# Optimization experiments

Hardware: AMD Instinct MI355X
Metric: run time of the kernel (lower is better)

The kernel has to match this reference:

```python
import jax, jax.numpy as jnp
import numpy as np
from jax import lax

B, T, HID = 2, 2048, 2048
H, DK, DV = 16, 64, 128          # num_heads, head_k_dim, head_v_dim
C = 16                            # chunk_size (hardcoded in module __call__)
LOWR = 16                         # gate_low_rank_dim
NORMALIZER = 16.0                 # gate_logit_normalizer
EPS = 1e-5
SCALE = DK ** -0.5


def setup_inputs() -> dict:
    key = jax.random.key(0)
    ks = jax.random.split(key, 9)
    def w(k, shape):
        return jax.random.normal(k, shape, jnp.float32) * (shape[0] ** -0.5)
    return {
        "hidden_states": jax.random.normal(ks[0], (B, T, HID), jnp.float32),
        "Wq": w(ks[1], (HID, H * DK)),
        "Wk": w(ks[2], (HID, H * DK)),
        "Wv": w(ks[3], (HID, H * DV)),
        "Wg": w(ks[4], (HID, H * DV)),
        "Wgk1": w(ks[5], (HID, LOWR)),
        "Wgk2": w(ks[6], (LOWR, H * DK)),
        "bgk2": jnp.zeros((H * DK,), jnp.float32),
        "Wo": w(ks[7], (H * DV, HID)),
        "norm_w": jnp.ones((DV,), jnp.float32),
    }


def _chunk_gla(q, k, v, gk):
    """Chunked gated linear attention.
    q,k,gk: [B,T,H,DK], v: [B,T,H,DV]; gk is log-decay (<= 0).
    Recurrence: S_t = diag(exp(gk_t)) S_{t-1} + k_t^T v_t ; o_t = scale * q_t S_t.
    """
    b, t, h, dk = q.shape
    dv = v.shape[-1]
    n = t // C
    def to_chunks(x):  # [B,T,H,d] -> [B,H,N,C,d]
        return x.reshape(b, n, C, h, x.shape[-1]).transpose(0, 3, 1, 2, 4)
    q, k, v, gk = map(to_chunks, (q, k, v, gk))

    gc = jnp.cumsum(gk, axis=3)                 # within-chunk cumulative log-decay
    qe = q * jnp.exp(gc) * SCALE                # decay-weighted queries
    ke = k * jnp.exp(-gc)                       # inverse-decay keys (safe for C=16)
    # intra-chunk causal attention: A[i,j] = sum_d q_i k_j exp(gc_i - gc_j), j<=i
    A = jnp.einsum('bhncd,bhnmd->bhncm', qe, ke)
    A = jnp.where(jnp.tril(jnp.ones((C, C), bool)), A, 0.0)
    o_intra = jnp.einsum('bhncm,bhnme->bhnce', A, v)

    g_last = gc[:, :, :, -1:, :]                # [B,H,N,1,DK]
    k_dec = k * jnp.exp(g_last - gc)            # keys decayed to end of chunk
    kv = jnp.einsum('bhncd,bhnce->bhnde', k_dec, v)   # per-chunk state increment
    decay = jnp.exp(g_last[:, :, :, 0, :])      # [B,H,N,DK] total chunk decay

    def step(S, inp):  # S: [B,H,DK,DV]
        qe_c, kv_c, dec_c = inp
        o_c = jnp.einsum('bhcd,bhde->bhce', qe_c, S)
        return dec_c[..., None] * S + kv_c, o_c

    S0 = jnp.zeros((b, h, dk, dv), q.dtype)
    xs = (qe.transpose(2, 0, 1, 3, 4), kv.transpose(2, 0, 1, 3, 4), decay.transpose(2, 0, 1, 3))
    _, o_inter = lax.scan(step, S0, xs)          # [N,B,H,C,DV]

    o = o_intra + o_inter.transpose(1, 2, 0, 3, 4)
    return o.transpose(0, 2, 3, 1, 4).reshape(b, t, h, dv)  # [B,T,H,DV]


def reference(hidden_states, Wq, Wk, Wv, Wg, Wgk1, Wgk2, bgk2, Wo, norm_w):
    x = hidden_states
    q = (x @ Wq).reshape(B, T, H, DK)
    k = (x @ Wk).reshape(B, T, H, DK)
    v = (x @ Wv).reshape(B, T, H, DV)
    gk = jax.nn.log_sigmoid((x @ Wgk1) @ Wgk2 + bgk2) / NORMALIZER
    gk = gk.reshape(B, T, H, DK)

    o = _chunk_gla(q, k, v, gk)                  # [B,T,H,DV]

    # FusedRMSNormGated: rmsnorm(o) * weight, gated by swish(g) per head
    g = (x @ Wg).reshape(B, T, H, DV)
    o = o * lax.rsqrt(jnp.mean(o * o, axis=-1, keepdims=True) + EPS) * norm_w
    o = o * (g * jax.nn.sigmoid(g))
    return o.reshape(B, T, H * DV) @ Wo
```

## Files before the change

kernel.cpp:

```cpp
#include <hip/hip_runtime.h>
#include <hip/hip_bf16.h>
#include <math.h>

#define B_    2
#define T_    2048
#define HID_  2048
#define H_    16
#define DK_   64
#define DV_   128
#define CC    16
#define NCHUNK (T_/CC)
#define NSEG  16
#define M_    (B_*T_)
#define SCALE_ 0.125f

typedef __attribute__((ext_vector_type(8))) __bf16 bf16x8;
typedef __attribute__((ext_vector_type(4))) float f32x4;

__device__ __forceinline__ unsigned short f2bf(float f) {
  unsigned int u = __float_as_uint(f);
  u += 0x7fff + ((u >> 16) & 1);
  return (unsigned short)(u >> 16);
}
__device__ __forceinline__ float bf2f(unsigned short u) {
  return __uint_as_float(((unsigned int)u) << 16);
}

typedef const __attribute__((address_space(1))) void* as1cv;
typedef __attribute__((address_space(3))) void* as3v;
__device__ __forceinline__ void gload16(const void* g, void* l) {
  __builtin_amdgcn_global_load_lds((as1cv)g, (as3v)l, 16, 0, 0);
}

__global__ __launch_bounds__(256) void prep_kernel(const float* __restrict__ x,
                                                   unsigned short* __restrict__ xb,
                                                   const float* __restrict__ Wq,
                                                   const float* __restrict__ Wk,
                                                   const float* __restrict__ Wv,
                                                   const float* __restrict__ Wg,
                                                   const float* __restrict__ Wo,
                                                   unsigned short* __restrict__ WqkT,
                                                   unsigned short* __restrict__ WvgT,
                                                   unsigned short* __restrict__ WoT) {
  int id = blockIdx.x;
  if (id < 8192) {
    int i = id * 256 + threadIdx.x;
    float4 f = reinterpret_cast<const float4*>(x)[i];
    ushort4 u;
    u.x = f2bf(f.x); u.y = f2bf(f.y); u.z = f2bf(f.z); u.w = f2bf(f.w);
    reinterpret_cast<ushort4*>(xb)[i] = u;
    return;
  }
  id -= 8192;
  const float* in; unsigned short* out; int N;
  if (id < 2048)       { in = Wq; out = WqkT;                         N = 1024; }
  else if (id < 4096)  { in = Wk; out = WqkT + (size_t)1024*2048;     N = 1024; id -= 2048; }
  else if (id < 8192)  { in = Wv; out = WvgT;                         N = 2048; id -= 4096; }
  else if (id < 12288) { in = Wg; out = WvgT + (size_t)2048*2048;     N = 2048; id -= 8192; }
  else                 { in = Wo; out = WoT;                          N = 2048; id -= 12288; }
  const int K = 2048;
  const int nx = N / 32;
  const int n0 = (id % nx) * 32;
  const int k0 = (id / nx) * 32;
  __shared__ float tile[32][33];
  const int tx = threadIdx.x & 31;
  const int ty = threadIdx.x >> 5;
  #pragma unroll
  for (int i = 0; i < 4; ++i)
    tile[ty + i*8][tx] = in[(size_t)(k0 + ty + i*8) * N + n0 + tx];
  __syncthreads();
  #pragma unroll
  for (int i = 0; i < 4; ++i) {
    int r = ty + i*8;
    out[(size_t)(n0 + r) * K + k0 + tx] = f2bf(tile[tx][r]);
  }
}

template<bool OBF>
__global__ __launch_bounds__(512, 2) void gemm256(const unsigned short* __restrict__ A,
                                                  const unsigned short* __restrict__ Bt,
                                                  void* __restrict__ Cv,
                                                  int M, int N, int K) {
  __shared__ char ldsb[131072];
  const int t    = threadIdx.x;
  const int lane = t & 63;
  const int wid  = t >> 6;
  const int wr   = wid >> 2;
  const int wc   = wid & 3;
  const int lr   = lane & 15;
  const int lk   = lane >> 4;
  int flat = blockIdx.y * gridDim.x + blockIdx.x;
  if (gridDim.x * gridDim.y == 256) flat = (flat & 7) * 32 + (flat >> 3);
  const int row0 = (flat / gridDim.x) * 256;
  const int col0 = (flat % gridDim.x) * 256;
  const int NKT  = K >> 6;
  const size_t K2 = (size_t)K * 2;

  const int r_s  = t >> 2;
  const int kx_s = ((t & 3) * 16) ^ (((t >> 5) & 1) << 5);

  const int ha = wr;
  const int hb = wc >> 1;
  const int rbl = (wc & 1) * 64;

  f32x4 acc[8][4];
  #pragma unroll
  for (int m = 0; m < 8; ++m)
    #pragma unroll
    for (int n = 0; n < 4; ++n) acc[m][n] = (f32x4){0.f, 0.f, 0.f, 0.f};

  auto stage_half = [&](int p, int o, int h, int kt) {
    const char* src = o ? (const char*)Bt : (const char*)A;
    const int R0 = (o ? col0 : row0) + h * 128;
    const char* g = src + (size_t)(R0 + r_s) * K2 + (size_t)kt * 128 + kx_s;
    char* l = ldsb + ((((p << 1) | o) << 1 | h) << 14) + t * 16;
    gload16(g, l);
    gload16(g + 64, l + 8192);
  };
  auto lda = [&](int p, int mf, int ks) -> bf16x8 {
    int r = mf * 16 + lr;
    int a = ((((p << 1) | 0) << 1 | ha) << 14) + ks * 8192 + r * 64 + lk * 16;
    a ^= ((r >> 3) & 1) << 5;
    return *(const bf16x8*)(ldsb + a);
  };
  auto ldb = [&](int p, int nf, int ks) -> bf16x8 {
    int r = rbl + nf * 16 + lr;
    int a = ((((p << 1) | 1) << 1 | hb) << 14) + ks * 8192 + r * 64 + lk * 16;
    a ^= ((r >> 3) & 1) << 5;
    return *(const bf16x8*)(ldsb + a);
  };

  stage_half(0, 1, 0, 0); stage_half(0, 1, 1, 0);
  stage_half(0, 0, 0, 0); stage_half(0, 0, 1, 0);
  if (1 < NKT) {
    stage_half(1, 1, 0, 1); stage_half(1, 1, 1, 1);
    stage_half(1, 0, 0, 1); stage_half(1, 0, 1, 1);
  }
  __builtin_amdgcn_sched_barrier(0);
  asm volatile("s_waitcnt vmcnt(8)" ::: "memory");
  __builtin_amdgcn_sched_barrier(0);
  __builtin_amdgcn_s_barrier();

  bf16x8 fa[4][2], fb[2][2], fb2[2][2];

  for (int kt = 0; kt < NKT; ++kt) {
    const int p = kt & 1;
    const bool st = (kt + 2 < NKT);
    #pragma unroll
    for (int m = 0; m < 4; ++m) { fa[m][0] = lda(p, m, 0); fa[m][1] = lda(p, m, 1); }
    #pragma unroll
    for (int n = 0; n < 2; ++n) { fb[n][0] = ldb(p, n, 0); fb[n][1] = ldb(p, n, 1); }
    __builtin_amdgcn_sched_barrier(0);
    __builtin_amdgcn_s_barrier();
    asm volatile("s_waitcnt lgkmcnt(0)" ::: "memory");
    __builtin_amdgcn_sched_barrier(0);
    __builtin_amdgcn_s_setprio(1);
    #pragma unroll
    for (int m = 0; m < 4; ++m)
      #pragma unroll
      for (int n = 0; n < 2; ++n) {
        acc[m][n] = __builtin_amdgcn_mfma_f32_16x16x32_bf16(fa[m][0], fb[n][0], acc[m][n], 0, 0, 0);
        acc[m][n] = __builtin_amdgcn_mfma_f32_16x16x32_bf16(fa[m][1], fb[n][1], acc[m][n], 0, 0, 0);
      }
    __builtin_amdgcn_s_setprio(0);
    __builtin_amdgcn_sched_barrier(0);
    __builtin_amdgcn_s_barrier();
    #pragma unroll
    for (int n = 0; n < 2; ++n) { fb2[n][0] = ldb(p, n + 2, 0); fb2[n][1] = ldb(p, n + 2, 1); }
    __builtin_amdgcn_sched_barrier(0);
    __builtin_amdgcn_s_barrier();
    asm volatile("s_waitcnt lgkmcnt(0)" ::: "memory");
    __builtin_amdgcn_sched_barrier(0);
    __builtin_amdgcn_s_setprio(1);
    #pragma unroll
    for (int m = 0; m < 4; ++m)
      #pragma unroll
      for (int n = 0; n < 2; ++n) {
        acc[m][n+2] = __builtin_amdgcn_mfma_f32_16x16x32_bf16(fa[m][0], fb2[n][0], acc[m][n+2], 0, 0, 0);
        acc[m][n+2] = __builtin_amdgcn_mfma_f32_16x16x32_bf16(fa[m][1], fb2[n][1], acc[m][n+2], 0, 0, 0);
      }
    __builtin_amdgcn_s_setprio(0);
    __builtin_amdgcn_sched_barrier(0);
    __builtin_amdgcn_s_barrier();
    if (st) { stage_half(p, 1, 0, kt + 2); stage_half(p, 1, 1, kt + 2); }
    #pragma unroll
    for (int m = 0; m < 4; ++m) { fa[m][0] = lda(p, m + 4, 0); fa[m][1] = lda(p, m + 4, 1); }
    __builtin_amdgcn_sched_barrier(0);
    __builtin_amdgcn_s_barrier();
    asm volatile("s_waitcnt lgkmcnt(0)" ::: "memory");
    __builtin_amdgcn_sched_barrier(0);
    __builtin_amdgcn_s_setprio(1);
    #pragma unroll
    for (int m = 0; m < 4; ++m)
      #pragma unroll
      for (int n = 0; n < 2; ++n) {
        acc[m+4][n] = __builtin_amdgcn_mfma_f32_16x16x32_bf16(fa[m][0], fb[n][0], acc[m+4][n], 0, 0, 0);
        acc[m+4][n] = __builtin_amdgcn_mfma_f32_16x16x32_bf16(fa[m][1], fb[n][1], acc[m+4][n], 0, 0, 0);
      }
    __builtin_amdgcn_s_setprio(0);
    __builtin_amdgcn_sched_barrier(0);
    __builtin_amdgcn_s_barrier();
    if (st) { stage_half(p, 0, 0, kt + 2); stage_half(p, 0, 1, kt + 2); }
    __builtin_amdgcn_sched_barrier(0);
    __builtin_amdgcn_s_setprio(1);
    #pragma unroll
    for (int m = 0; m < 4; ++m)
      #pragma unroll
      for (int n = 0; n < 2; ++n) {
        acc[m+4][n+2] = __builtin_amdgcn_mfma_f32_16x16x32_bf16(fa[m][0], fb2[n][0], acc[m+4][n+2], 0, 0, 0);
        acc[m+4][n+2] = __builtin_amdgcn_mfma_f32_16x16x32_bf16(fa[m][1], fb2[n][1], acc[m+4][n+2], 0, 0, 0);
      }
    __builtin_amdgcn_s_setprio(0);
    __builtin_amdgcn_sched_barrier(0);
    if (kt == NKT - 2) asm volatile("s_waitcnt vmcnt(0)" ::: "memory");
    else               asm volatile("s_waitcnt vmcnt(8)" ::: "memory");
    __builtin_amdgcn_sched_barrier(0);
    __builtin_amdgcn_s_barrier();
  }

  #pragma unroll
  for (int m = 0; m < 8; ++m) {
    int row = row0 + wr*128 + m*16 + lk*4;
    #pragma unroll
    for (int n = 0; n < 4; ++n) {
      int col = col0 + wc*64 + n*16 + lr;
      #pragma unroll
      for (int j = 0; j < 4; ++j) {
        if (OBF) ((unsigned short*)Cv)[(size_t)(row + j) * N + col] = f2bf(acc[m][n][j]);
        else     ((float*)Cv)[(size_t)(row + j) * N + col] = acc[m][n][j];
      }
    }
  }
}

template<bool OBF>
__global__ __launch_bounds__(512, 2) void gemm256x128(const unsigned short* __restrict__ A,
                                                      const unsigned short* __restrict__ Bt,
                                                      void* __restrict__ Cv,
                                                      int M, int N, int K) {
  __shared__ char ldsb[98304];
  const int t    = threadIdx.x;
  const int lane = t & 63;
  const int wid  = t >> 6;
  const int wr   = wid >> 1;
  const int wc   = wid & 1;
  const int lr   = lane & 15;
  const int lk   = lane >> 4;
  int flat = blockIdx.y * gridDim.x + blockIdx.x;
  if (gridDim.x * gridDim.y == 256) flat = (flat & 7) * 32 + (flat >> 3);
  const int row0 = (flat / gridDim.x) * 256;
  const int col0 = (flat % gridDim.x) * 128;
  const int NKT  = K >> 6;
  const size_t K2 = (size_t)K * 2;

  const int r_s  = t >> 2;
  const int kx_s = ((t & 3) * 16) ^ (((t >> 5) & 1) << 5);

  const int ha  = wr >> 1;
  const int ral = (wr & 1) * 64;
  const int rbl = wc * 64;

  f32x4 acc[4][4];
  #pragma unroll
  for (int m = 0; m < 4; ++m)
    #pragma unroll
    for (int n = 0; n < 4; ++n) acc[m][n] = (f32x4){0.f, 0.f, 0.f, 0.f};

  auto stage_slot = [&](int p, int slot, int kt) {
    const char* src = (slot == 2) ? (const char*)Bt : (const char*)A;
    const int R0 = (slot == 2) ? col0 : (row0 + slot * 128);
    const char* g = src + (size_t)(R0 + r_s) * K2 + (size_t)kt * 128 + kx_s;
    char* l = ldsb + p * 49152 + slot * 16384 + t * 16;
    gload16(g, l);
    gload16(g + 64, l + 8192);
  };
  auto lda = [&](int p, int mf, int ks) -> bf16x8 {
    int r = ral + mf * 16 + lr;
    int a = p * 49152 + ha * 16384 + ks * 8192 + r * 64 + lk * 16;
    a ^= ((r >> 3) & 1) << 5;
    return *(const bf16x8*)(ldsb + a);
  };
  auto ldb = [&](int p, int nf, int ks) -> bf16x8 {
    int r = rbl + nf * 16 + lr;
    int a = p * 49152 + 32768 + ks * 8192 + r * 64 + lk * 16;
    a ^= ((r >> 3) & 1) << 5;
    return *(const bf16x8*)(ldsb + a);
  };

  stage_slot(0, 2, 0); stage_slot(0, 0, 0); stage_slot(0, 1, 0);
  if (1 < NKT) { stage_slot(1, 2, 1); stage_slot(1, 0, 1); stage_slot(1, 1, 1); }
  __builtin_amdgcn_sched_barrier(0);
  asm volatile("s_waitcnt vmcnt(6)" ::: "memory");
  __builtin_amdgcn_sched_barrier(0);
  __builtin_amdgcn_s_barrier();

  bf16x8 fa[2][2], fa2[2][2], fb[2][2], fb2[2][2];

  for (int kt = 0; kt < NKT; ++kt) {
    const int p = kt & 1;
    const bool st = (kt + 2 < NKT);
    #pragma unroll
    for (int m = 0; m < 2; ++m) { fa[m][0] = lda(p, m, 0); fa[m][1] = lda(p, m, 1); }
    #pragma unroll
    for (int n = 0; n < 2; ++n) { fb[n][0] = ldb(p, n, 0); fb[n][1] = ldb(p, n, 1); }
    __builtin_amdgcn_sched_barrier(0);
    __builtin_amdgcn_s_barrier();
    asm volatile("s_waitcnt lgkmcnt(0)" ::: "memory");
    __builtin_amdgcn_sched_barrier(0);
    __builtin_amdgcn_s_setprio(1);
    #pragma unroll
    for (int m = 0; m < 2; ++m)
      #pragma unroll
      for (int n = 0; n < 2; ++n) {
        acc[m][n] = __builtin_amdgcn_mfma_f32_16x16x32_bf16(fa[m][0], fb[n][0], acc[m][n], 0, 0, 0);
        acc[m][n] = __builtin_amdgcn_mfma_f32_16x16x32_bf16(fa[m][1], fb[n][1], acc[m][n], 0, 0, 0);
      }
    __builtin_amdgcn_s_setprio(0);
    __builtin_amdgcn_sched_barrier(0);
    __builtin_amdgcn_s_barrier();
    #pragma unroll
    for (int n = 0; n < 2; ++n) { fb2[n][0] = ldb(p, n + 2, 0); fb2[n][1] = ldb(p, n + 2, 1); }
    __builtin_amdgcn_sched_barrier(0);
    __builtin_amdgcn_s_barrier();
    asm volatile("s_waitcnt lgkmcnt(0)" ::: "memory");
    __builtin_amdgcn_sched_barrier(0);
    __builtin_amdgcn_s_setprio(1);
    #pragma unroll
    for (int m = 0; m < 2; ++m)
      #pragma unroll
      for (int n = 0; n < 2; ++n) {
        acc[m][n+2] = __builtin_amdgcn_mfma_f32_16x16x32_bf16(fa[m][0], fb2[n][0], acc[m][n+2], 0, 0, 0);
        acc[m][n+2] = __builtin_amdgcn_mfma_f32_16x16x32_bf16(fa[m][1], fb2[n][1], acc[m][n+2], 0, 0, 0);
      }
    __builtin_amdgcn_s_setprio(0);
    __builtin_amdgcn_sched_barrier(0);
    __builtin_amdgcn_s_barrier();
    if (st) stage_slot(p, 2, kt + 2);
    #pragma unroll
    for (int m = 0; m < 2; ++m) { fa2[m][0] = lda(p, m + 2, 0); fa2[m][1] = lda(p, m + 2, 1); }
    __builtin_amdgcn_sched_barrier(0);
    __builtin_amdgcn_s_barrier();
    asm volatile("s_waitcnt lgkmcnt(0)" ::: "memory");
    __builtin_amdgcn_sched_barrier(0);
    __builtin_amdgcn_s_setprio(1);
    #pragma unroll
    for (int m = 0; m < 2; ++m)
      #pragma unroll
      for (int n = 0; n < 2; ++n) {
        acc[m+2][n] = __builtin_amdgcn_mfma_f32_16x16x32_bf16(fa2[m][0], fb[n][0], acc[m+2][n], 0, 0, 0);
        acc[m+2][n] = __builtin_amdgcn_mfma_f32_16x16x32_bf16(fa2[m][1], fb[n][1], acc[m+2][n], 0, 0, 0);
      }
    __builtin_amdgcn_s_setprio(0);
    __builtin_amdgcn_sched_barrier(0);
    __builtin_amdgcn_s_barrier();
    if (st) { stage_slot(p, 0, kt + 2); stage_slot(p, 1, kt + 2); }
    __builtin_amdgcn_sched_barrier(0);
    __builtin_amdgcn_s_setprio(1);
    #pragma unroll
    for (int m = 0; m < 2; ++m)
      #pragma unroll
      for (int n = 0; n < 2; ++n) {
        acc[m+2][n+2] = __builtin_amdgcn_mfma_f32_16x16x32_bf16(fa2[m][0], fb2[n][0], acc[m+2][n+2], 0, 0, 0);
        acc[m+2][n+2] = __builtin_amdgcn_mfma_f32_16x16x32_bf16(fa2[m][1], fb2[n][1], acc[m+2][n+2], 0, 0, 0);
      }
    __builtin_amdgcn_s_setprio(0);
    __builtin_amdgcn_sched_barrier(0);
    if (kt == NKT - 2) asm volatile("s_waitcnt vmcnt(0)" ::: "memory");
    else               asm volatile("s_waitcnt vmcnt(6)" ::: "memory");
    __builtin_amdgcn_sched_barrier(0);
    __builtin_amdgcn_s_barrier();
  }

  #pragma unroll
  for (int m = 0; m < 4; ++m) {
    int row = row0 + wr*64 + m*16 + lk*4;
    #pragma unroll
    for (int n = 0; n < 4; ++n) {
      int col = col0 + wc*64 + n*16 + lr;
      #pragma unroll
      for (int j = 0; j < 4; ++j) {
        if (OBF) ((unsigned short*)Cv)[(size_t)(row + j) * N + col] = f2bf(acc[m][n][j]);
        else     ((float*)Cv)[(size_t)(row + j) * N + col] = acc[m][n][j];
      }
    }
  }
}

__global__ __launch_bounds__(256) void lr_kernel(const float* __restrict__ x,
                                                 const float* __restrict__ w1,
                                                 const float* __restrict__ w2,
                                                 const float* __restrict__ bias,
                                                 float* __restrict__ gkout) {
  __shared__ float part[16][17];
  __shared__ float tr[16];
  const int row = blockIdx.x;
  const int j = threadIdx.x & 15;
  const int p = threadIdx.x >> 4;
  const float* xr = x + (size_t)row * HID_;
  float acc = 0.f;
  const int k0 = p * 128;
  for (int kk = k0; kk < k0 + 128; kk += 4) {
    float4 xv = *reinterpret_cast<const float4*>(&xr[kk]);
    acc = fmaf(xv.x, w1[(kk+0)*16 + j], acc);
    acc = fmaf(xv.y, w1[(kk+1)*16 + j], acc);
    acc = fmaf(xv.z, w1[(kk+2)*16 + j], acc);
    acc = fmaf(xv.w, w1[(kk+3)*16 + j], acc);
  }
  part[p][j] = acc;
  __syncthreads();
  if (threadIdx.x < 16) {
    float s = 0.f;
    #pragma unroll
    for (int pp = 0; pp < 16; ++pp) s += part[pp][threadIdx.x];
    tr[threadIdx.x] = s;
  }
  __syncthreads();
  for (int n = threadIdx.x; n < H_*DK_; n += 256) {
    float a2 = bias[n];
    #pragma unroll
    for (int jj = 0; jj < 16; ++jj) a2 = fmaf(tr[jj], w2[jj * (H_*DK_) + n], a2);
    float ls = fminf(a2, 0.f) - log1pf(expf(-fabsf(a2)));
    gkout[(size_t)row * (H_*DK_) + n] = ls * (1.f / 16.f);
  }
}

__global__ __launch_bounds__(256) void gla_phase_a(const float* __restrict__ qk,
                                                   const unsigned short* __restrict__ vg,
                                                   const float* __restrict__ gk,
                                                   float* __restrict__ Sseg,
                                                   float* __restrict__ Dseg) {
  const int seg = blockIdx.x & 15;
  const int h   = (blockIdx.x >> 4) & 15;
  const int b   = blockIdx.x >> 8;
  const int t    = threadIdx.x;
  const int lane = t & 63;
  const int wid  = t >> 6;
  const int q    = lane >> 4;
  const int lr   = lane & 15;
  __shared__ float gc[16][68];
  __shared__ float dec_[64];
  __shared__ unsigned short kdT[64][40];
  __shared__ unsigned short vvT[128][40];

  for (int i = t; i < 1024; i += 256) kdT[i >> 4][16 + (i & 15)] = 0;
  for (int i = t; i < 2048; i += 256) vvT[i >> 4][16 + (i & 15)] = 0;

  f32x4 s_reg[2][4];
  #pragma unroll
  for (int et = 0; et < 2; ++et)
    #pragma unroll
    for (int dt = 0; dt < 4; ++dt) s_reg[et][dt] = (f32x4){0.f,0.f,0.f,0.f};
  float gt = 0.f;

  for (int c8 = 0; c8 < NCHUNK/NSEG; ++c8) {
    const int ch = seg * (NCHUNK/NSEG) + c8;
    __syncthreads();
    {
      float acc = 0.f;
      #pragma unroll
      for (int c = 0; c < CC; ++c) {
        acc += gk[((size_t)(b*T_ + ch*CC + c)) * 1024 + h*DK_ + lane];
        gc[c][lane] = acc;
      }
      gt += acc;
      dec_[lane] = expf(acc);
    }
    __syncthreads();
    {
      int c = t >> 4, d0 = (t & 15) * 4;
      float4 k4 = *reinterpret_cast<const float4*>(
          &qk[((size_t)(b*T_ + ch*CC + c)) * 2048 + 1024 + h*DK_ + d0]);
      float ka[4] = {k4.x, k4.y, k4.z, k4.w};
      #pragma unroll
      for (int j = 0; j < 4; ++j)
        kdT[d0 + j][c] = f2bf(ka[j] * expf(gc[CC-1][d0 + j] - gc[c][d0 + j]));
    }
    {
      int c = t & 15, e0 = (t >> 4) * 8;
      const ushort4* vp = reinterpret_cast<const ushort4*>(
          &vg[((size_t)(b*T_ + ch*CC + c)) * 4096 + h*DV_ + e0]);
      ushort4 a = vp[0], bb = vp[1];
      vvT[e0+0][c] = a.x;  vvT[e0+1][c] = a.y;  vvT[e0+2][c] = a.z;  vvT[e0+3][c] = a.w;
      vvT[e0+4][c] = bb.x; vvT[e0+5][c] = bb.y; vvT[e0+6][c] = bb.z; vvT[e0+7][c] = bb.w;
    }
    __syncthreads();
    bf16x8 vf[2], kf[4];
    #pragma unroll
    for (int et = 0; et < 2; ++et)
      vf[et] = *(const bf16x8*)&vvT[wid*32 + et*16 + lr][q*8];
    #pragma unroll
    for (int dt = 0; dt < 4; ++dt)
      kf[dt] = *(const bf16x8*)&kdT[dt*16 + lr][q*8];
    #pragma unroll
    for (int et = 0; et < 2; ++et)
      #pragma unroll
      for (int dt = 0; dt < 4; ++dt) {
        f32x4 dl = __builtin_amdgcn_mfma_f32_16x16x32_bf16(vf[et], kf[dt],
                     (f32x4){0.f,0.f,0.f,0.f}, 0, 0, 0);
        float dv = dec_[dt*16 + lr];
        #pragma unroll
        for (int j = 0; j < 4; ++j)
          s_reg[et][dt][j] = fmaf(s_reg[et][dt][j], dv, dl[j]);
      }
  }
  const size_t base = ((size_t)((b*H_ + h)*NSEG + seg)) * (DK_*DV_);
  #pragma unroll
  for (int et = 0; et < 2; ++et)
    #pragma unroll
    for (int dt = 0; dt < 4; ++dt)
      #pragma unroll
      for (int j = 0; j < 4; ++j)
        Sseg[base + (size_t)(wid*32 + et*16 + q*4 + j) * 64 + dt*16 + lr] = s_reg[et][dt][j];
  if (t < 64)
    Dseg[(size_t)((b*H_ + h)*NSEG + seg) * DK_ + t] = expf(gt);
}

__global__ __launch_bounds__(256) void gla_combine(float* __restrict__ Sseg,
                                                   const float* __restrict__ Dseg) {
  const int bh = blockIdx.x;
  const int t = threadIdx.x;
  __shared__ float Dl[64];
  float4 S_run[8];
  #pragma unroll
  for (int j = 0; j < 8; ++j) S_run[j] = (float4){0.f,0.f,0.f,0.f};
  const int d0 = (t * 4) & 63;
  for (int seg = 0; seg < NSEG; ++seg) {
    const size_t base = ((size_t)bh*NSEG + seg) * (DK_*DV_);
    if (t < 64) Dl[t] = Dseg[((size_t)bh*NSEG + seg) * DK_ + t];
    __syncthreads();
    #pragma unroll
    for (int j = 0; j < 8; ++j) {
      int idx = j*1024 + t*4;
      float4 sl = *reinterpret_cast<float4*>(&Sseg[base + idx]);
      *reinterpret_cast<float4*>(&Sseg[base + idx]) = S_run[j];
      S_run[j].x = fmaf(Dl[d0+0], S_run[j].x, sl.x);
      S_run[j].y = fmaf(Dl[d0+1], S_run[j].y, sl.y);
      S_run[j].z = fmaf(Dl[d0+2], S_run[j].z, sl.z);
      S_run[j].w = fmaf(Dl[d0+3], S_run[j].w, sl.w);
    }
    __syncthreads();
  }
}

__global__ __launch_bounds__(256) void gla_phase_c(const float* __restrict__ qk,
                                                   const unsigned short* __restrict__ vg,
                                                   const float* __restrict__ gk,
                                                   const float* __restrict__ Sseg,
                                                   const float* __restrict__ norm_w,
                                                   unsigned short* __restrict__ yb) {
  const int seg = blockIdx.x & 15;
  const int h   = (blockIdx.x >> 4) & 15;
  const int b   = blockIdx.x >> 8;
  const int t    = threadIdx.x;
  const int lane = t & 63;
  const int wid  = t >> 6;
  const int q    = lane >> 4;
  const int lr   = lane & 15;
  __shared__ float gc[16][68];
  __shared__ float dec_[64];
  __shared__ unsigned short qe[16][72];
  __shared__ unsigned short ke[16][72];
  __shared__ unsigned short kdT[64][40];
  __shared__ unsigned short vvT[128][40];
  __shared__ unsigned short Am[16][40];
  __shared__ unsigned short Sb[128][72];
  __shared__ float ss_lds[4][16];
  __shared__ float nw[128];

  for (int i = t; i < 1024; i += 256) kdT[i >> 4][16 + (i & 15)] = 0;
  for (int i = t; i < 2048; i += 256) vvT[i >> 4][16 + (i & 15)] = 0;
  if (t < 256) { int c = t >> 4, m = t & 15; Am[c][16 + m] = 0; }
  if (t < 128) nw[t] = norm_w[t];

  f32x4 s_reg[2][4];
  const size_t sbase = ((size_t)((b*H_ + h)*NSEG + seg)) * (DK_*DV_);
  #pragma unroll
  for (int et = 0; et < 2; ++et)
    #pragma unroll
    for (int dt = 0; dt < 4; ++dt)
      #pragma unroll
      for (int j = 0; j < 4; ++j) {
        int e = wid*32 + et*16 + q*4 + j, d = dt*16 + lr;
        float v = Sseg[sbase + (size_t)e * 64 + d];
        s_reg[et][dt][j] = v;
        Sb[e][d] = f2bf(v);
      }

  for (int c8 = 0; c8 < NCHUNK/NSEG; ++c8) {
    const int ch = seg * (NCHUNK/NSEG) + c8;
    __syncthreads();
    {
      float acc = 0.f;
      #pragma unroll
      for (int c = 0; c < CC; ++c) {
        acc += gk[((size_t)(b*T_ + ch*CC + c)) * 1024 + h*DK_ + lane];
        gc[c][lane] = acc;
      }
      dec_[lane] = expf(acc);
    }
    __syncthreads();
    {
      int c = t >> 4, d0 = (t & 15) * 4;
      const size_t gbq = ((size_t)(b*T_ + ch*CC + c)) * 2048 + h*DK_ + d0;
      float4 q4 = *reinterpret_cast<const float4*>(&qk[gbq]);
      float4 k4 = *reinterpret_cast<const float4*>(&qk[gbq + 1024]);
      float qa[4] = {q4.x, q4.y, q4.z, q4.w};
      float ka[4] = {k4.x, k4.y, k4.z, k4.w};
      ushort4 qw, kw;
      unsigned short* qwp = (unsigned short*)&qw;
      unsigned short* kwp = (unsigned short*)&kw;
      #pragma unroll
      for (int j = 0; j < 4; ++j) {
        float gcv = gc[c][d0 + j];
        float gl  = gc[CC-1][d0 + j];
        qwp[j] = f2bf(qa[j] * expf(gcv) * SCALE_);
        kwp[j] = f2bf(ka[j] * expf(-gcv));
        kdT[d0 + j][c] = f2bf(ka[j] * expf(gl - gcv));
      }
      *reinterpret_cast<ushort4*>(&qe[c][d0]) = qw;
      *reinterpret_cast<ushort4*>(&ke[c][d0]) = kw;
    }
    {
      int c = t & 15, e0 = (t >> 4) * 8;
      const ushort4* vp = reinterpret_cast<const ushort4*>(
          &vg[((size_t)(b*T_ + ch*CC + c)) * 4096 + h*DV_ + e0]);
      ushort4 a = vp[0], bb = vp[1];
      vvT[e0+0][c] = a.x;  vvT[e0+1][c] = a.y;  vvT[e0+2][c] = a.z;  vvT[e0+3][c] = a.w;
      vvT[e0+4][c] = bb.x; vvT[e0+5][c] = bb.y; vvT[e0+6][c] = bb.z; vvT[e0+7][c] = bb.w;
    }
    __syncthreads();
    bf16x8 qA0 = *(const bf16x8*)&qe[lr][q*8];
    bf16x8 qA1 = *(const bf16x8*)&qe[lr][32 + q*8];
    {
      bf16x8 kB0 = *(const bf16x8*)&ke[lr][q*8];
      bf16x8 kB1 = *(const bf16x8*)&ke[lr][32 + q*8];
      f32x4 accA = __builtin_amdgcn_mfma_f32_16x16x32_bf16(qA0, kB0,
                     (f32x4){0.f,0.f,0.f,0.f}, 0, 0, 0);
      accA = __builtin_amdgcn_mfma_f32_16x16x32_bf16(qA1, kB1, accA, 0, 0, 0);
      #pragma unroll
      for (int j = 0; j < 4; ++j) {
        int c = q*4 + j;
        Am[c][lr] = (lr <= c) ? f2bf(accA[j]) : (unsigned short)0;
      }
    }
    bf16x8 vf[2], kf[4];
    #pragma unroll
    for (int et = 0; et < 2; ++et)
      vf[et] = *(const bf16x8*)&vvT[wid*32 + et*16 + lr][q*8];
    #pragma unroll
    for (int dt = 0; dt < 4; ++dt)
      kf[dt] = *(const bf16x8*)&kdT[dt*16 + lr][q*8];
    #pragma unroll
    for (int et = 0; et < 2; ++et)
      #pragma unroll
      for (int dt = 0; dt < 4; ++dt) {
        f32x4 dl = __builtin_amdgcn_mfma_f32_16x16x32_bf16(vf[et], kf[dt],
                     (f32x4){0.f,0.f,0.f,0.f}, 0, 0, 0);
        float dv = dec_[dt*16 + lr];
        #pragma unroll
        for (int j = 0; j < 4; ++j)
          s_reg[et][dt][j] = fmaf(s_reg[et][dt][j], dv, dl[j]);
      }
    __syncthreads();
    {
      bf16x8 amA = *(const bf16x8*)&Am[lr][q*8];
      f32x4 accO[2];
      #pragma unroll
      for (int et = 0; et < 2; ++et) {
        int e0 = wid*32 + et*16;
        bf16x8 sB0 = *(const bf16x8*)&Sb[e0 + lr][q*8];
        bf16x8 sB1 = *(const bf16x8*)&Sb[e0 + lr][32 + q*8];
        accO[et] = __builtin_amdgcn_mfma_f32_16x16x32_bf16(qA0, sB0,
                     (f32x4){0.f,0.f,0.f,0.f}, 0, 0, 0);
        accO[et] = __builtin_amdgcn_mfma_f32_16x16x32_bf16(qA1, sB1, accO[et], 0, 0, 0);
        accO[et] = __builtin_amdgcn_mfma_f32_16x16x32_bf16(amA, vf[et], accO[et], 0, 0, 0);
      }
      #pragma unroll
      for (int j = 0; j < 4; ++j) {
        float pj = accO[0][j]*accO[0][j] + accO[1][j]*accO[1][j];
        pj += __shfl_xor(pj, 1, 64);
        pj += __shfl_xor(pj, 2, 64);
        pj += __shfl_xor(pj, 4, 64);
        pj += __shfl_xor(pj, 8, 64);
        if (lr == 0) ss_lds[wid][q*4 + j] = pj;
      }
      __syncthreads();
      #pragma unroll
      for (int j = 0; j < 4; ++j) {
        int r = q*4 + j;
        float tot = ss_lds[0][r] + ss_lds[1][r] + ss_lds[2][r] + ss_lds[3][r];
        float inv = rsqrtf(tot * (1.f/128.f) + 1e-5f);
        const size_t rowg = (size_t)(b*T_ + ch*CC + r);
        #pragma unroll
        for (int et = 0; et < 2; ++et) {
          int e = wid*32 + et*16 + lr;
          float gv = bf2f(vg[rowg * 4096 + 2048 + h*DV_ + e]);
          float si = gv / (1.f + expf(-gv));
          yb[rowg * 2048 + h*DV_ + e] = f2bf(accO[et][j] * inv * nw[e] * si);
        }
      }
    }
    __syncthreads();
    #pragma unroll
    for (int et = 0; et < 2; ++et)
      #pragma unroll
      for (int dt = 0; dt < 4; ++dt)
        #pragma unroll
        for (int j = 0; j < 4; ++j)
          Sb[wid*32 + et*16 + q*4 + j][dt*16 + lr] = f2bf(s_reg[et][dt][j]);
  }
}

extern "C" void kernel_launch(void* const* d_in, const int* in_sizes, int n_in,
                              void* d_out, int out_size, void* d_ws, size_t ws_size,
                              hipStream_t stream) {
  const float* x      = (const float*)d_in[0];
  const float* Wq     = (const float*)d_in[1];
  const float* Wk     = (const float*)d_in[2];
  const float* Wv     = (const float*)d_in[3];
  const float* Wg     = (const float*)d_in[4];
  const float* Wgk1   = (const float*)d_in[5];
  const float* Wgk2   = (const float*)d_in[6];
  const float* bgk2   = (const float*)d_in[7];
  const float* Wo     = (const float*)d_in[8];
  const float* norm_w = (const float*)d_in[9];
  float* out = (float*)d_out;
  float* ws  = (float*)d_ws;

  float*          qk   = ws;
  float*          gkb  = ws + 8388608;
  unsigned short* vg   = (unsigned short*)(ws + 12582912);
  float*          wbuf = ws + 20971520;
  float*          Sseg = ws + 29360128;
  float*          Dseg = ws + 33554432;
  unsigned short* WoT  = (unsigned short*)(ws + 33652736);

  unsigned short* xb   = (unsigned short*)gkb;
  unsigned short* WqkT = (unsigned short*)wbuf;
  unsigned short* WvgT = (unsigned short*)(wbuf + 2097152);
  unsigned short* yb   = (unsigned short*)wbuf;

  dim3 blk(256);
  prep_kernel<<<dim3(24576), blk, 0, stream>>>(x, xb, Wq, Wk, Wv, Wg, Wo, WqkT, WvgT, WoT);
  gemm256x128<false><<<dim3(2048/128, 4096/256), dim3(512), 0, stream>>>(xb, WqkT, qk, M_, 2048, HID_);
  gemm256<true     ><<<dim3(4096/256, 4096/256), dim3(512), 0, stream>>>(xb, WvgT, vg, M_, 4096, HID_);
  lr_kernel<<<M_, blk, 0, stream>>>(x, Wgk1, Wgk2, bgk2, gkb);
  gla_phase_a<<<B_*H_*NSEG, blk, 0, stream>>>(qk, vg, gkb, Sseg, Dseg);
  gla_combine<<<B_*H_, blk, 0, stream>>>(Sseg, Dseg);
  gla_phase_c<<<B_*H_*NSEG, blk, 0, stream>>>(qk, vg, gkb, Sseg, norm_w, yb);
  gemm256x128<false><<<dim3(2048/128, 4096/256), dim3(512), 0, stream>>>(yb, WoT, out, M_, HID_, HID_);
}
```

Before: 296.3 us.

## Fuse low-rank gate kernel into prep and tighten GEMM barrier schedule

The low-rank gate projection (lr_kernel) is merged into the prep kernel as extra blocks, which saves a launch and lets that work overlap with the conversions and transposes. xb is moved out of the gkb buffer so both can be written in the same kernel. In both GEMM kernels the fb2 LDS reads are issued earlier under a partial lgkmcnt wait, several s_barriers are removed, and MFMA groups are merged so fewer synchronization points split the compute. Removing barriers risks LDS read/write hazards with the double-buffered staging if the reordering is not exactly right.

Result: no change. 296.5 us (+0.1%).

```diff
diff --git a/kernel.cpp b/kernel.cpp
--- a/kernel.cpp
+++ b/kernel.cpp
@@ -41,7 +41,14 @@
                                                    const float* __restrict__ Wo,
                                                    unsigned short* __restrict__ WqkT,
                                                    unsigned short* __restrict__ WvgT,
-                                                   unsigned short* __restrict__ WoT) {
+                                                   unsigned short* __restrict__ WoT,
+                                                   const float* __restrict__ w1,
+                                                   const float* __restrict__ w2,
+                                                   const float* __restrict__ bias,
+                                                   float* __restrict__ gkout) {
+  __shared__ float tile[32][33];
+  __shared__ float part[16][17];
+  __shared__ float tr[16];
   int id = blockIdx.x;
   if (id < 8192) {
     int i = id * 256 + threadIdx.x;
@@ -49,6 +56,38 @@
     ushort4 u;
     u.x = f2bf(f.x); u.y = f2bf(f.y); u.z = f2bf(f.z); u.w = f2bf(f.w);
     reinterpret_cast<ushort4*>(xb)[i] = u;
+    return;
+  }
+  if (id >= 24576) {
+    const int row = id - 24576;
+    const int j = threadIdx.x & 15;
+    const int p = threadIdx.x >> 4;
+    const float* xr = x + (size_t)row * HID_;
+    float acc = 0.f;
+    const int k0 = p * 128;
+    for (int kk = k0; kk < k0 + 128; kk += 4) {
+      float4 xv = *reinterpret_cast<const float4*>(&xr[kk]);
+      acc = fmaf(xv.x, w1[(kk+0)*16 + j], acc);
+      acc = fmaf(xv.y, w1[(kk+1)*16 + j], acc);
+      acc = fmaf(xv.z, w1[(kk+2)*16 + j], acc);
+      acc = fmaf(xv.w, w1[(kk+3)*16 + j], acc);
+    }
+    part[p][j] = acc;
+    __syncthreads();
+    if (threadIdx.x < 16) {
+      float s = 0.f;
+      #pragma unroll
+      for (int pp = 0; pp < 16; ++pp) s += part[pp][threadIdx.x];
+      tr[threadIdx.x] = s;
+    }
+    __syncthreads();
+    for (int n = threadIdx.x; n < H_*DK_; n += 256) {
+      float a2 = bias[n];
+      #pragma unroll
+      for (int jj = 0; jj < 16; ++jj) a2 = fmaf(tr[jj], w2[jj * (H_*DK_) + n], a2);
+      float ls = fminf(a2, 0.f) - log1pf(expf(-fabsf(a2)));
+      gkout[(size_t)row * (H_*DK_) + n] = ls * (1.f / 16.f);
+    }
     return;
   }
   id -= 8192;
@@ -62,7 +101,6 @@
   const int nx = N / 32;
   const int n0 = (id % nx) * 32;
   const int k0 = (id / nx) * 32;
-  __shared__ float tile[32][33];
   const int tx = threadIdx.x & 31;
   const int ty = threadIdx.x >> 5;
   #pragma unroll
@@ -148,11 +186,14 @@
     const bool st = (kt + 2 < NKT);
     #pragma unroll
     for (int m = 0; m < 4; ++m) { fa[m][0] = lda(p, m, 0); fa[m][1] = lda(p, m, 1); }
+    __builtin_amdgcn_sched_barrier(0);
     #pragma unroll
     for (int n = 0; n < 2; ++n) { fb[n][0] = ldb(p, n, 0); fb[n][1] = ldb(p, n, 1); }
     __builtin_amdgcn_sched_barrier(0);
-    __builtin_amdgcn_s_barrier();
-    asm volatile("s_waitcnt lgkmcnt(0)" ::: "memory");
+    #pragma unroll
+    for (int n = 0; n < 2; ++n) { fb2[n][0] = ldb(p, n + 2, 0); fb2[n][1] = ldb(p, n + 2, 1); }
+    __builtin_amdgcn_sched_barrier(0);
+    asm volatile("s_waitcnt lgkmcnt(4)" ::: "memory");
     __builtin_amdgcn_sched_barrier(0);
     __builtin_amdgcn_s_setprio(1);
     #pragma unroll
@@ -164,11 +205,6 @@
       }
     __builtin_amdgcn_s_setprio(0);
     __builtin_amdgcn_sched_barrier(0);
-    __builtin_amdgcn_s_barrier();
-    #pragma unroll
-    for (int n = 0; n < 2; ++n) { fb2[n][0] = ldb(p, n + 2, 0); fb2[n][1] = ldb(p, n + 2, 1); }
-    __builtin_amdgcn_sched_barrier(0);
-    __builtin_amdgcn_s_barrier();
     asm volatile("s_waitcnt lgkmcnt(0)" ::: "memory");
     __builtin_amdgcn_sched_barrier(0);
     __builtin_amdgcn_s_setprio(1);
@@ -183,10 +219,10 @@
     __builtin_amdgcn_sched_barrier(0);
     __builtin_amdgcn_s_barrier();
     if (st) { stage_half(p, 1, 0, kt + 2); stage_half(p, 1, 1, kt + 2); }
+    __builtin_amdgcn_sched_barrier(0);
     #pragma unroll
     for (int m = 0; m < 4; ++m) { fa[m][0] = lda(p, m + 4, 0); fa[m][1] = lda(p, m + 4, 1); }
     __builtin_amdgcn_sched_barrier(0);
-    __builtin_amdgcn_s_barrier();
     asm volatile("s_waitcnt lgkmcnt(0)" ::: "memory");
     __builtin_amdgcn_sched_barrier(0);
     __builtin_amdgcn_s_setprio(1);
@@ -197,12 +233,6 @@
         acc[m+4][n] = __builtin_amdgcn_mfma_f32_16x16x32_bf16(fa[m][0], fb[n][0], acc[m+4][n], 0, 0, 0);
         acc[m+4][n] = __builtin_amdgcn_mfma_f32_16x16x32_bf16(fa[m][1], fb[n][1], acc[m+4][n], 0, 0, 0);
       }
-    __builtin_amdgcn_s_setprio(0);
-    __builtin_amdgcn_sched_barrier(0);
-    __builtin_amdgcn_s_barrier();
-    if (st) { stage_half(p, 0, 0, kt + 2); stage_half(p, 0, 1, kt + 2); }
-    __builtin_amdgcn_sched_barrier(0);
-    __builtin_amdgcn_s_setprio(1);
     #pragma unroll
     for (int m = 0; m < 4; ++m)
       #pragma unroll
@@ -211,6 +241,9 @@
         acc[m+4][n+2] = __builtin_amdgcn_mfma_f32_16x16x32_bf16(fa[m][1], fb2[n][1], acc[m+4][n+2], 0, 0, 0);
       }
     __builtin_amdgcn_s_setprio(0);
+    __builtin_amdgcn_sched_barrier(0);
+    __builtin_amdgcn_s_barrier();
+    if (st) { stage_half(p, 0, 0, kt + 2); stage_half(p, 0, 1, kt + 2); }
     __builtin_amdgcn_sched_barrier(0);
     if (kt == NKT - 2) asm volatile("s_waitcnt vmcnt(0)" ::: "memory");
     else               asm volatile("s_waitcnt vmcnt(8)" ::: "memory");
@@ -294,18 +327,21 @@
   __builtin_amdgcn_sched_barrier(0);
   __builtin_amdgcn_s_barrier();
 
-  bf16x8 fa[2][2], fa2[2][2], fb[2][2], fb2[2][2];
+  bf16x8 fa[2][2], fb[2][2], fb2[2][2];
 
   for (int kt = 0; kt < NKT; ++kt) {
     const int p = kt & 1;
     const bool st = (kt + 2 < NKT);
     #pragma unroll
     for (int m = 0; m < 2; ++m) { fa[m][0] = lda(p, m, 0); fa[m][1] = lda(p, m, 1); }
+    __builtin_amdgcn_sched_barrier(0);
     #pragma unroll
     for (int n = 0; n < 2; ++n) { fb[n][0] = ldb(p, n, 0); fb[n][1] = ldb(p, n, 1); }
     __builtin_amdgcn_sched_barrier(0);
-    __builtin_amdgcn_s_barrier();
-    asm volatile("s_waitcnt lgkmcnt(0)" ::: "memory");
+    #pragma unroll
+    for (int n = 0; n < 2; ++n) { fb2[n][0] = ldb(p, n + 2, 0); fb2[n][1] = ldb(p, n + 2, 1); }
+    __builtin_amdgcn_sched_barrier(0);
+    asm volatile("s_waitcnt lgkmcnt(4)" ::: "memory");
     __builtin_amdgcn_sched_barrier(0);
     __builtin_amdgcn_s_setprio(1);
     #pragma unroll
@@ -317,11 +353,6 @@
       }
     __builtin_amdgcn_s_setprio(0);
     __builtin_amdgcn_sched_barrier(0);
-    __builtin_amdgcn_s_barrier();
-    #pragma unroll
-    for (int n = 0; n < 2; ++n) { fb2[n][0] = ldb(p, n + 2, 0); fb2[n][1] = ldb(p, n + 2, 1); }
-    __builtin_amdgcn_sched_barrier(0);
-    __builtin_amdgcn_s_barrier();
     asm volatile("s_waitcnt lgkmcnt(0)" ::: "memory");
     __builtin_amdgcn_sched_barrier(0);
     __builtin_amdgcn_s_setprio(1);
@@ -336,10 +367,10 @@
     __builtin_amdgcn_sched_barrier(0);
     __builtin_amdgcn_s_barrier();
     if (st) stage_slot(p, 2, kt + 2);
-    #pragma unroll
-    for (int m = 0; m < 2; ++m) { fa2[m][0] = lda(p, m + 2, 0); fa2[m][1] = lda(p, m + 2, 1); }
-    __builtin_amdgcn_sched_barrier(0);
-    __builtin_amdgcn_s_barrier();
+    __builtin_amdgcn_sched_barrier(0);
+    #pragma unroll
+    for (int m = 0; m < 2; ++m) { fa[m][0] = lda(p, m + 2, 0); fa[m][1] = lda(p, m + 2, 1); }
+    __builtin_amdgcn_sched_barrier(0);
     asm volatile("s_waitcnt lgkmcnt(0)" ::: "memory");
     __builtin_amdgcn_sched_barrier(0);
     __builtin_amdgcn_s_setprio(1);
@@ -347,23 +378,20 @@
     for (int m = 0; m < 2; ++m)
       #pragma unroll
       for (int n = 0; n < 2; ++n) {
-        acc[m+2][n] = __builtin_amdgcn_mfma_f32_16x16x32_bf16(fa2[m][0], fb[n][0], acc[m+2][n], 0, 0, 0);
-        acc[m+2][n] = __builtin_amdgcn_mfma_f32_16x16x32_bf16(fa2[m][1], fb[n][1], acc[m+2][n], 0, 0, 0);
+        acc[m+2][n] = __builtin_amdgcn_mfma_f32_16x16x32_bf16(fa[m][0], fb[n][0], acc[m+2][n], 0, 0, 0);
+        acc[m+2][n] = __builtin_amdgcn_mfma_f32_16x16x32_bf16(fa[m][1], fb[n][1], acc[m+2][n], 0, 0, 0);
+      }
+    #pragma unroll
+    for (int m = 0; m < 2; ++m)
+      #pragma unroll
+      for (int n = 0; n < 2; ++n) {
+        acc[m+2][n+2] = __builtin_amdgcn_mfma_f32_16x16x32_bf16(fa[m][0], fb2[n][0], acc[m+2][n+2], 0, 0, 0);
+        acc[m+2][n+2] = __builtin_amdgcn_mfma_f32_16x16x32_bf16(fa[m][1], fb2[n][1], acc[m+2][n+2], 0, 0, 0);
       }
     __builtin_amdgcn_s_setprio(0);
     __builtin_amdgcn_sched_barrier(0);
     __builtin_amdgcn_s_barrier();
     if (st) { stage_slot(p, 0, kt + 2); stage_slot(p, 1, kt + 2); }
-    __builtin_amdgcn_sched_barrier(0);
-    __builtin_amdgcn_s_setprio(1);
-    #pragma unroll
-    for (int m = 0; m < 2; ++m)
-      #pragma unroll
-      for (int n = 0; n < 2; ++n) {
-        acc[m+2][n+2] = __builtin_amdgcn_mfma_f32_16x16x32_bf16(fa2[m][0], fb2[n][0], acc[m+2][n+2], 0, 0, 0);
-        acc[m+2][n+2] = __builtin_amdgcn_mfma_f32_16x16x32_bf16(fa2[m][1], fb2[n][1], acc[m+2][n+2], 0, 0, 0);
-      }
-    __builtin_amdgcn_s_setprio(0);
     __builtin_amdgcn_sched_barrier(0);
     if (kt == NKT - 2) asm volatile("s_waitcnt vmcnt(0)" ::: "memory");
     else               asm volatile("s_waitcnt vmcnt(6)" ::: "memory");
@@ -383,44 +411,6 @@
         else     ((float*)Cv)[(size_t)(row + j) * N + col] = acc[m][n][j];
       }
     }
-  }
-}
-
-__global__ __launch_bounds__(256) void lr_kernel(const float* __restrict__ x,
-                                                 const float* __restrict__ w1,
-                                                 const float* __restrict__ w2,
-                                                 const float* __restrict__ bias,
-                                                 float* __restrict__ gkout) {
-  __shared__ float part[16][17];
-  __shared__ float tr[16];
-  const int row = blockIdx.x;
-  const int j = threadIdx.x & 15;
-  const int p = threadIdx.x >> 4;
-  const float* xr = x + (size_t)row * HID_;
-  float acc = 0.f;
-  const int k0 = p * 128;
-  for (int kk = k0; kk < k0 + 128; kk += 4) {
-    float4 xv = *reinterpret_cast<const float4*>(&xr[kk]);
-    acc = fmaf(xv.x, w1[(kk+0)*16 + j], acc);
-    acc = fmaf(xv.y, w1[(kk+1)*16 + j], acc);
-    acc = fmaf(xv.z, w1[(kk+2)*16 + j], acc);
-    acc = fmaf(xv.w, w1[(kk+3)*16 + j], acc);
-  }
-  part[p][j] = acc;
-  __syncthreads();
-  if (threadIdx.x < 16) {
-    float s = 0.f;
-    #pragma unroll
-    for (int pp = 0; pp < 16; ++pp) s += part[pp][threadIdx.x];
-    tr[threadIdx.x] = s;
-  }
-  __syncthreads();
-  for (int n = threadIdx.x; n < H_*DK_; n += 256) {
-    float a2 = bias[n];
-    #pragma unroll
-    for (int jj = 0; jj < 16; ++jj) a2 = fmaf(tr[jj], w2[jj * (H_*DK_) + n], a2);
-    float ls = fminf(a2, 0.f) - log1pf(expf(-fabsf(a2)));
-    gkout[(size_t)row * (H_*DK_) + n] = ls * (1.f / 16.f);
   }
 }
 
@@ -738,13 +728,15 @@
   unsigned short* xb   = (unsigned short*)gkb;
   unsigned short* WqkT = (unsigned short*)wbuf;
   unsigned short* WvgT = (unsigned short*)(wbuf + 2097152);
-  unsigned short* yb   = (unsigned short*)wbuf;
+  xb                   = (unsigned short*)(wbuf + 6291456);
+  unsigned short* yb   = (unsigned short*)ws;
+  yb                   = (unsigned short*)wbuf;
 
   dim3 blk(256);
-  prep_kernel<<<dim3(24576), blk, 0, stream>>>(x, xb, Wq, Wk, Wv, Wg, Wo, WqkT, WvgT, WoT);
+  prep_kernel<<<dim3(28672), blk, 0, stream>>>(x, xb, Wq, Wk, Wv, Wg, Wo, WqkT, WvgT, WoT,
+                                               Wgk1, Wgk2, bgk2, gkb);
   gemm256x128<false><<<dim3(2048/128, 4096/256), dim3(512), 0, stream>>>(xb, WqkT, qk, M_, 2048, HID_);
   gemm256<true     ><<<dim3(4096/256, 4096/256), dim3(512), 0, stream>>>(xb, WvgT, vg, M_, 4096, HID_);
-  lr_kernel<<<M_, blk, 0, stream>>>(x, Wgk1, Wgk2, bgk2, gkb);
   gla_phase_a<<<B_*H_*NSEG, blk, 0, stream>>>(qk, vg, gkb, Sseg, Dseg);
   gla_combine<<<B_*H_, blk, 0, stream>>>(Sseg, Dseg);
   gla_phase_c<<<B_*H_*NSEG, blk, 0, stream>>>(qk, vg, gkb, Sseg, norm_w, yb);
```
